# Performance work log

Hardware: AMD Instinct MI355X
Metric: run time of the kernel (lower is better)

The kernel has to match this reference:

```python
import jax, jax.numpy as jnp
import numpy as np
from jax import lax

I, H, O, L = 8, 50, 6, 3
B, T = 4096, 256


def setup_inputs() -> dict:
    key = jax.random.key(0)
    ks = jax.random.split(key, 16)
    s = 1.0 / np.sqrt(H)  # PyTorch LSTM init scale
    inp = {"x": jax.random.normal(ks[0], (B, T, I), dtype=jnp.float32)}
    in_dims = [I, H, H]
    ki = 1
    for l in range(L):
        inp[f"w_ih{l}"] = jax.random.uniform(ks[ki], (4 * H, in_dims[l]), minval=-s, maxval=s); ki += 1
        inp[f"w_hh{l}"] = jax.random.uniform(ks[ki], (4 * H, H), minval=-s, maxval=s); ki += 1
        inp[f"b_ih{l}"] = jax.random.uniform(ks[ki], (4 * H,), minval=-s, maxval=s); ki += 1
        inp[f"b_hh{l}"] = jax.random.uniform(ks[ki], (4 * H,), minval=-s, maxval=s); ki += 1
    inp["w_fc"] = jax.random.uniform(ks[13], (O, H), minval=-s, maxval=s)
    inp["b_fc"] = jax.random.uniform(ks[14], (O,), minval=-s, maxval=s)
    return inp


def _lstm_layer(x, w_ih, w_hh, b_ih, b_hh):
    # x: [B, T, in]; returns [B, T, H]. PyTorch gate order: i, f, g, o.
    b = b_ih + b_hh
    pre = jnp.einsum('bti,gi->btg', x, w_ih) + b  # input projections for all steps at once
    h0 = jnp.zeros((x.shape[0], H), x.dtype)
    c0 = jnp.zeros((x.shape[0], H), x.dtype)

    def step(carry, p_t):
        h, c = carry
        gates = p_t + h @ w_hh.T
        i, f, g, o = jnp.split(gates, 4, axis=-1)
        i = jax.nn.sigmoid(i); f = jax.nn.sigmoid(f)
        g = jnp.tanh(g); o = jax.nn.sigmoid(o)
        c = f * c + i * g
        h = o * jnp.tanh(c)
        return (h, c), h

    (_, _), hs = lax.scan(step, (h0, c0), jnp.swapaxes(pre, 0, 1))  # [T, B, H]
    return jnp.swapaxes(hs, 0, 1)


def reference(x, w_ih0, w_hh0, b_ih0, b_hh0, w_ih1, w_hh1, b_ih1, b_hh1,
              w_ih2, w_hh2, b_ih2, b_hh2, w_fc, b_fc):
    h = _lstm_layer(x, w_ih0, w_hh0, b_ih0, b_hh0)
    h = _lstm_layer(h, w_ih1, w_hh1, b_ih1, b_hh1)
    h = _lstm_layer(h, w_ih2, w_hh2, b_ih2, b_hh2)
    last = h[:, -1, :]  # [B, H]
    return last @ w_fc.T + b_fc  # [B, O]
```

## Files before the change

### kernel.cpp

```cpp
#include <hip/hip_runtime.h>
#include <hip/hip_bf16.h>
#include <cstddef>


#define T_STEPS 256
#define BTOT    4096
#define NTHR    768

typedef __attribute__((ext_vector_type(8))) short short8;
typedef __attribute__((ext_vector_type(4))) float f32x4;

#define BAR() do { \
    asm volatile("s_waitcnt lgkmcnt(0)" ::: "memory"); \
    __builtin_amdgcn_sched_barrier(0); \
    __builtin_amdgcn_s_barrier(); \
    __builtin_amdgcn_sched_barrier(0); \
} while (0)

__device__ __forceinline__ float fast_sigmoid(float x) {
    float e = __builtin_amdgcn_exp2f(-1.4426950408889634f * x);
    return __builtin_amdgcn_rcpf(1.0f + e);
}
__device__ __forceinline__ float fast_tanh(float x) {
    float e = __builtin_amdgcn_exp2f(2.8853900817779268f * x);
    return 1.0f - 2.0f * __builtin_amdgcn_rcpf(1.0f + e);
}
__device__ __forceinline__ unsigned short f2bf(float x) {
    union { __hip_bfloat16 b; unsigned short s; } u;
    u.b = __float2bfloat16(x);
    return u.s;
}
__device__ __forceinline__ float bf2f(unsigned short s) {
    union { unsigned u; float f; } v; v.u = (unsigned)s << 16; return v.f;
}
__device__ __forceinline__ float cell_upd(f32x4 g, float& cst) {
    float ig = fast_sigmoid(g[0]);
    float fg = fast_sigmoid(g[1]);
    float gg = fast_tanh(g[2]);
    float og = fast_sigmoid(g[3]);
    float c  = fmaf(fg, cst, ig * gg);
    cst = c;
    return og * fast_tanh(c);
}

template<int NT, int KS, int XK, int BIASK>
__device__ __forceinline__ void load_wb(int T0, int lane,
    const float* __restrict__ w_ih, const float* __restrict__ w_hh,
    const float* __restrict__ b_ih, const float* __restrict__ b_hh,
    short8 (&Wh)[NT][KS], short8 (&Wl)[NT][KS])
{
    const int m = lane & 15, kg = lane >> 4;
    #pragma unroll
    for (int q = 0; q < NT; ++q) {
        int gp = (T0 + q) * 16 + m;
        int gr = (gp < 200) ? ((gp & 3) * 50 + (gp >> 2)) : -1;
        #pragma unroll
        for (int ks = 0; ks < KS; ++ks)
            #pragma unroll
            for (int e = 0; e < 8; ++e) {
                int k = ks * 32 + kg * 8 + e;
                float v = 0.0f;
                if (gr >= 0) {
                    if (k < XK) v = w_ih[gr * XK + k];
                    else if (k < XK + 50) v = w_hh[gr * 50 + (k - XK)];
                    else if (k == BIASK) v = b_ih[gr] + b_hh[gr];
                }
                unsigned short hb = f2bf(v);
                Wh[q][ks][e] = (short)hb;
                Wl[q][ks][e] = (short)f2bf(v - bf2f(hb));
            }
    }
}

template<int NT, int KS, int HK, bool WRB, bool LASTL>
__device__ __forceinline__ void step_body(
    int t, int T0, int lane,
    const short* Arh,
    short* Awh,
    short* Axh,
    float* hfp,
    const short8 (&Wh)[NT][KS], const short8 (&Wl)[NT][KS],
    float (&cst)[NT])
{
    const int b = lane & 15, kg = lane >> 4;

    short8 Ah[KS];
    #pragma unroll
    for (int ks = 0; ks < KS; ++ks)
        Ah[ks] = *(const short8*)&Arh[(ks * 4 + kg) * 128 + b * 8];

    f32x4 acc[NT];
    #pragma unroll
    for (int q = 0; q < NT; ++q) acc[q] = (f32x4){0.0f, 0.0f, 0.0f, 0.0f};

    #pragma unroll
    for (int ks = 0; ks < KS; ++ks)
        #pragma unroll
        for (int q = 0; q < NT; ++q)
            acc[q] = __builtin_amdgcn_mfma_f32_16x16x32_bf16(Wh[q][ks], Ah[ks], acc[q], 0, 0, 0);
    #pragma unroll
    for (int ks = 0; ks < KS; ++ks)
        #pragma unroll
        for (int q = 0; q < NT; ++q)
            acc[q] = __builtin_amdgcn_mfma_f32_16x16x32_bf16(Wl[q][ks], Ah[ks], acc[q], 0, 0, 0);

    #pragma unroll
    for (int q = 0; q < NT; ++q) {
        int n = (T0 + q) * 4 + kg;
        if (n < 50) {
            float h = cell_upd(acc[q], cst[q]);
            unsigned short hb = f2bf(h);
            int k  = HK + n;
            Awh[(k >> 3) * 128 + b * 8 + (k & 7)] = (short)hb;
            if (WRB)
                Axh[(n >> 3) * 128 + b * 8 + (n & 7)] = (short)hb;
            if (LASTL && t == T_STEPS - 1) hfp[b * 56 + n] = h;
        }
    }
}

template<int NT, bool XST>
__device__ void role_l0(int T0, int lane, int b0, const float* __restrict__ xf,
    const float* w_ih, const float* w_hh, const float* b_ih, const float* b_hh,
    short (*A0h)[1024], short (*A1h)[2048])
{
    short8 Wh[NT][2], Wl[NT][2];
    load_wb<NT, 2, 8, 58>(T0, lane, w_ih, w_hh, b_ih, b_hh, Wh, Wl);
    float cst[NT];
    #pragma unroll
    for (int q = 0; q < NT; ++q) cst[q] = 0.0f;
    const int bb = lane & 15, kg = lane >> 4;

    for (int it = 0; it < T_STEPS + 2; ++it) {
        const bool stg = XST && (kg == 0) && (it + 1 < T_STEPS);
        float xs[8];
        if (stg) {
            const float* xr = &xf[((size_t)(b0 + bb) * T_STEPS + (it + 1)) * 8];
            *(float4*)&xs[0] = *(const float4*)xr;
            *(float4*)&xs[4] = *(const float4*)(xr + 4);
        }
        if (it < T_STEPS) {
            int cur = it & 1, nxt = cur ^ 1;
            step_body<NT, 2, 8, true, false>(it, T0, lane,
                A0h[cur], A0h[nxt], A1h[cur], nullptr, Wh, Wl, cst);
        }
        if (stg) {
            int nb = (it + 1) & 1;
            short8 hi;
            #pragma unroll
            for (int e = 0; e < 8; ++e) hi[e] = (short)f2bf(xs[e]);
            *(short8*)&A0h[nb][bb * 8] = hi;
        }
        BAR();
    }
}

template<bool LASTL>
__device__ void role_mid(int T0, int lane,
    const float* w_ih, const float* w_hh, const float* b_ih, const float* b_hh,
    short (*Arh)[2048], short (*Axh)[2048], float* hfp)
{
    constexpr int SKEW = LASTL ? 2 : 1;
    short8 Wh[3][4], Wl[3][4];
    load_wb<3, 4, 50, 100>(T0, lane, w_ih, w_hh, b_ih, b_hh, Wh, Wl);
    float cst[3] = {0.0f, 0.0f, 0.0f};

    for (int it = 0; it < T_STEPS + 2; ++it) {
        int t = it - SKEW;
        if (t >= 0 && t < T_STEPS) {
            step_body<3, 4, 50, !LASTL, LASTL>(t, T0, lane,
                Arh[t & 1], Arh[(t + 1) & 1],
                LASTL ? (short*)nullptr : Axh[t & 1],
                hfp, Wh, Wl, cst);
        }
        BAR();
    }
}

__device__ void role_orphan(int lane,
    const float* w_ih1, const float* w_hh1, const float* b_ih1, const float* b_hh1,
    const float* w_ih2, const float* w_hh2, const float* b_ih2, const float* b_hh2,
    short (*A1h)[2048], short (*A2h)[2048], float* hfp)
{
    short8 W1h[1][4], W1l[1][4], W2h[1][4], W2l[1][4];
    load_wb<1, 4, 50, 100>(12, lane, w_ih1, w_hh1, b_ih1, b_hh1, W1h, W1l);
    load_wb<1, 4, 50, 100>(12, lane, w_ih2, w_hh2, b_ih2, b_hh2, W2h, W2l);
    float c1 = 0.0f, c2 = 0.0f;
    const int b = lane & 15, kg = lane >> 4;

    for (int it = 0; it < T_STEPS + 2; ++it) {
        int t1 = it - 1, t2 = it - 2;
        bool d1 = (unsigned)t1 < T_STEPS, d2 = (unsigned)t2 < T_STEPS;

        short8 A1[4], A2[4];
        #pragma unroll
        for (int ks = 0; ks < 4; ++ks) {
            int ga = (ks * 4 + kg) * 128 + b * 8;
            if (d1) A1[ks] = *(const short8*)&A1h[t1 & 1][ga];
            if (d2) A2[ks] = *(const short8*)&A2h[t2 & 1][ga];
        }

        f32x4 a1 = (f32x4){0.0f, 0.0f, 0.0f, 0.0f};
        f32x4 a2 = (f32x4){0.0f, 0.0f, 0.0f, 0.0f};
        #pragma unroll
        for (int ks = 0; ks < 4; ++ks) {
            if (d1) a1 = __builtin_amdgcn_mfma_f32_16x16x32_bf16(W1h[0][ks], A1[ks], a1, 0, 0, 0);
            if (d2) a2 = __builtin_amdgcn_mfma_f32_16x16x32_bf16(W2h[0][ks], A2[ks], a2, 0, 0, 0);
        }
        #pragma unroll
        for (int ks = 0; ks < 4; ++ks) {
            if (d1) a1 = __builtin_amdgcn_mfma_f32_16x16x32_bf16(W1l[0][ks], A1[ks], a1, 0, 0, 0);
            if (d2) a2 = __builtin_amdgcn_mfma_f32_16x16x32_bf16(W2l[0][ks], A2[ks], a2, 0, 0, 0);
        }

        const int n = 48 + kg;
        if (d1 && kg < 2) {
            float h = cell_upd(a1, c1);
            unsigned short hb = f2bf(h);
            int k = 50 + n;
            A1h[(t1 + 1) & 1][(k >> 3) * 128 + b * 8 + (k & 7)] = (short)hb;
            A2h[t1 & 1][(n >> 3) * 128 + b * 8 + (n & 7)] = (short)hb;
        }
        if (d2 && kg < 2) {
            float h = cell_upd(a2, c2);
            unsigned short hb = f2bf(h);
            int k = 50 + n;
            A2h[(t2 + 1) & 1][(k >> 3) * 128 + b * 8 + (k & 7)] = (short)hb;
            if (t2 == T_STEPS - 1) hfp[b * 56 + n] = h;
        }
        BAR();
    }
}

__global__ __launch_bounds__(NTHR) void lstm_fused(
    const float* __restrict__ xf,
    const float* w_ih0, const float* w_hh0, const float* b_ih0, const float* b_hh0,
    const float* w_ih1, const float* w_hh1, const float* b_ih1, const float* b_hh1,
    const float* w_ih2, const float* w_hh2, const float* b_ih2, const float* b_hh2,
    const float* __restrict__ w_fc, const float* __restrict__ b_fc,
    float* __restrict__ out)
{
    __shared__ __align__(16) short A0h[2][1024];
    __shared__ __align__(16) short A1h[2][2048];
    __shared__ __align__(16) short A2h[2][2048];
    __shared__ __align__(16) float hf[16 * 56];

    const int tid  = threadIdx.x;
    const int lane = tid & 63;
    const int wid  = tid >> 6;
    const int b0   = blockIdx.x * 16;

    for (int i = tid; i < 2048; i += NTHR) ((short*)A0h)[i] = 0;
    for (int i = tid; i < 4096; i += NTHR) { ((short*)A1h)[i] = 0; ((short*)A2h)[i] = 0; }
    __syncthreads();

    if (tid < 32) {
        int buf = tid >> 4, b = tid & 15;
        A0h[buf][(58 >> 3) * 128 + b * 8 + (58 & 7)] = (short)0x3F80;
        A1h[buf][(100 >> 3) * 128 + b * 8 + (100 & 7)] = (short)0x3F80;
        A2h[buf][(100 >> 3) * 128 + b * 8 + (100 & 7)] = (short)0x3F80;
    }
    if (tid < 16) {
        int b = tid;
        #pragma unroll
        for (int j = 0; j < 8; ++j) {
            float v = xf[((size_t)(b0 + b) * T_STEPS + 0) * 8 + j];
            A0h[0][b * 8 + j] = (short)f2bf(v);
        }
    }
    __syncthreads();

    if      (wid == 0)  role_l0<5, false>(0, lane, b0, xf, w_ih0, w_hh0, b_ih0, b_hh0, A0h, A1h);
    else if (wid == 1)  role_l0<4, false>(5, lane, b0, xf, w_ih0, w_hh0, b_ih0, b_hh0, A0h, A1h);
    else if (wid == 2)  role_l0<4, true >(9, lane, b0, xf, w_ih0, w_hh0, b_ih0, b_hh0, A0h, A1h);
    else if (wid == 3)  role_mid<false>(0, lane, w_ih1, w_hh1, b_ih1, b_hh1, A1h, A2h, nullptr);
    else if (wid == 4)  role_mid<false>(3, lane, w_ih1, w_hh1, b_ih1, b_hh1, A1h, A2h, nullptr);
    else if (wid == 5)  role_mid<false>(6, lane, w_ih1, w_hh1, b_ih1, b_hh1, A1h, A2h, nullptr);
    else if (wid == 6)  role_mid<false>(9, lane, w_ih1, w_hh1, b_ih1, b_hh1, A1h, A2h, nullptr);
    else if (wid == 7)  role_mid<true >(0, lane, w_ih2, w_hh2, b_ih2, b_hh2, A2h, nullptr, hf);
    else if (wid == 8)  role_mid<true >(3, lane, w_ih2, w_hh2, b_ih2, b_hh2, A2h, nullptr, hf);
    else if (wid == 9)  role_mid<true >(6, lane, w_ih2, w_hh2, b_ih2, b_hh2, A2h, nullptr, hf);
    else if (wid == 10) role_mid<true >(9, lane, w_ih2, w_hh2, b_ih2, b_hh2, A2h, nullptr, hf);
    else                role_orphan(lane,
                            w_ih1, w_hh1, b_ih1, b_hh1,
                            w_ih2, w_hh2, b_ih2, b_hh2,
                            A1h, A2h, hf);

    __syncthreads();

    if (tid < 96) {
        int b = tid / 6, o = tid - b * 6;
        float a = b_fc[o];
        #pragma unroll
        for (int n = 0; n < 50; ++n)
            a = fmaf(w_fc[o * 50 + n], hf[b * 56 + n], a);
        out[(size_t)(b0 + b) * 6 + o] = a;
    }
}

extern "C" void kernel_launch(void* const* d_in, const int* in_sizes, int n_in,
                              void* d_out, int out_size, void* d_ws, size_t ws_size,
                              hipStream_t stream) {
    (void)in_sizes; (void)n_in; (void)d_ws; (void)ws_size; (void)out_size;

    const float* x     = (const float*)d_in[0];
    const float* w_ih0 = (const float*)d_in[1];
    const float* w_hh0 = (const float*)d_in[2];
    const float* b_ih0 = (const float*)d_in[3];
    const float* b_hh0 = (const float*)d_in[4];
    const float* w_ih1 = (const float*)d_in[5];
    const float* w_hh1 = (const float*)d_in[6];
    const float* b_ih1 = (const float*)d_in[7];
    const float* b_hh1 = (const float*)d_in[8];
    const float* w_ih2 = (const float*)d_in[9];
    const float* w_hh2 = (const float*)d_in[10];
    const float* b_ih2 = (const float*)d_in[11];
    const float* b_hh2 = (const float*)d_in[12];
    const float* w_fc  = (const float*)d_in[13];
    const float* b_fc  = (const float*)d_in[14];
    float* out = (float*)d_out;

    lstm_fused<<<dim3(BTOT / 16), dim3(NTHR), 0, stream>>>(
        x, w_ih0, w_hh0, b_ih0, b_hh0, w_ih1, w_hh1, b_ih1, b_hh1,
        w_ih2, w_hh2, b_ih2, b_hh2, w_fc, b_fc, out);
}
```

Baseline: 304.8 us.

## Single-buffer LDS state with two barriers per step and register prefetch of activations

Drops the double-buffered LDS state arrays for single buffers. Each timestep now uses two barriers: the first separates compute and writes, the second follows a register prefetch of the next step's inputs from LDS. The orphan warp now also takes one layer-0 gate tile, so layer 0 is split 4/4/4+1. The x staging is pipelined two steps ahead from global memory. This trades a second barrier per step for earlier LDS reads and halved LDS footprint, and the extra barrier may cost more than it saves.

```diff
diff --git a/kernel.cpp b/kernel.cpp
--- a/kernel.cpp
+++ b/kernel.cpp
@@ -72,37 +72,38 @@
     }
 }
 
-template<int NT, int KS, int HK, bool WRB, bool LASTL>
-__device__ __forceinline__ void step_body(
-    int t, int T0, int lane,
-    const short* Arh,
-    short* Awh,
-    short* Axh,
-    float* hfp,
+template<int KS>
+__device__ __forceinline__ void prefetch(const short* Ar, int lane, short8 (&Ap)[KS]) {
+    const int b = lane & 15, kg = lane >> 4;
+    #pragma unroll
+    for (int ks = 0; ks < KS; ++ks)
+        Ap[ks] = *(const short8*)&Ar[(ks * 4 + kg) * 128 + b * 8];
+}
+
+template<int T0, int NT, int KS, int HK, bool WRB, bool LASTL>
+__device__ __forceinline__ void compute_step(
+    int t, int lane,
+    short* Aw, short* Ax, float* hfp,
+    const short8 (&Ap)[KS],
     const short8 (&Wh)[NT][KS], const short8 (&Wl)[NT][KS],
     float (&cst)[NT])
 {
     const int b = lane & 15, kg = lane >> 4;
 
-    short8 Ah[KS];
+    f32x4 acc[NT];
+    #pragma unroll
+    for (int q = 0; q < NT; ++q) acc[q] = (f32x4){0.0f, 0.0f, 0.0f, 0.0f};
+
     #pragma unroll
     for (int ks = 0; ks < KS; ++ks)
-        Ah[ks] = *(const short8*)&Arh[(ks * 4 + kg) * 128 + b * 8];
-
-    f32x4 acc[NT];
-    #pragma unroll
-    for (int q = 0; q < NT; ++q) acc[q] = (f32x4){0.0f, 0.0f, 0.0f, 0.0f};
-
+        #pragma unroll
+        for (int q = 0; q < NT; ++q)
+            acc[q] = __builtin_amdgcn_mfma_f32_16x16x32_bf16(Wh[q][ks], Ap[ks], acc[q], 0, 0, 0);
     #pragma unroll
     for (int ks = 0; ks < KS; ++ks)
         #pragma unroll
         for (int q = 0; q < NT; ++q)
-            acc[q] = __builtin_amdgcn_mfma_f32_16x16x32_bf16(Wh[q][ks], Ah[ks], acc[q], 0, 0, 0);
-    #pragma unroll
-    for (int ks = 0; ks < KS; ++ks)
-        #pragma unroll
-        for (int q = 0; q < NT; ++q)
-            acc[q] = __builtin_amdgcn_mfma_f32_16x16x32_bf16(Wl[q][ks], Ah[ks], acc[q], 0, 0, 0);
+            acc[q] = __builtin_amdgcn_mfma_f32_16x16x32_bf16(Wl[q][ks], Ap[ks], acc[q], 0, 0, 0);
 
     #pragma unroll
     for (int q = 0; q < NT; ++q) {
@@ -110,124 +111,104 @@
         if (n < 50) {
             float h = cell_upd(acc[q], cst[q]);
             unsigned short hb = f2bf(h);
-            int k  = HK + n;
-            Awh[(k >> 3) * 128 + b * 8 + (k & 7)] = (short)hb;
+            int k = HK + n;
+            Aw[(k >> 3) * 128 + b * 8 + (k & 7)] = (short)hb;
             if (WRB)
-                Axh[(n >> 3) * 128 + b * 8 + (n & 7)] = (short)hb;
+                Ax[(n >> 3) * 128 + b * 8 + (n & 7)] = (short)hb;
             if (LASTL && t == T_STEPS - 1) hfp[b * 56 + n] = h;
         }
     }
 }
 
-template<int NT, bool XST>
-__device__ void role_l0(int T0, int lane, int b0, const float* __restrict__ xf,
+template<int T0, bool XST>
+__device__ void role_l0(int lane, int b0, const float* __restrict__ xf,
     const float* w_ih, const float* w_hh, const float* b_ih, const float* b_hh,
-    short (*A0h)[1024], short (*A1h)[2048])
-{
-    short8 Wh[NT][2], Wl[NT][2];
-    load_wb<NT, 2, 8, 58>(T0, lane, w_ih, w_hh, b_ih, b_hh, Wh, Wl);
-    float cst[NT];
-    #pragma unroll
-    for (int q = 0; q < NT; ++q) cst[q] = 0.0f;
+    short* A0, short* A1)
+{
+    short8 Wh[4][2], Wl[4][2];
+    load_wb<4, 2, 8, 58>(T0, lane, w_ih, w_hh, b_ih, b_hh, Wh, Wl);
+    float cst[4] = {0.0f, 0.0f, 0.0f, 0.0f};
+    short8 Ap[2];
     const int bb = lane & 15, kg = lane >> 4;
 
-    for (int it = 0; it < T_STEPS + 2; ++it) {
-        const bool stg = XST && (kg == 0) && (it + 1 < T_STEPS);
-        float xs[8];
-        if (stg) {
-            const float* xr = &xf[((size_t)(b0 + bb) * T_STEPS + (it + 1)) * 8];
-            *(float4*)&xs[0] = *(const float4*)xr;
-            *(float4*)&xs[4] = *(const float4*)(xr + 4);
+    float xp[2][8];
+    if (XST && kg == 0) {
+        #pragma unroll
+        for (int s = 0; s < 2; ++s) {
+            const float* xr = &xf[((size_t)(b0 + bb) * T_STEPS + (1 + s)) * 8];
+            *(float4*)&xp[s][0] = *(const float4*)xr;
+            *(float4*)&xp[s][4] = *(const float4*)(xr + 4);
         }
-        if (it < T_STEPS) {
-            int cur = it & 1, nxt = cur ^ 1;
-            step_body<NT, 2, 8, true, false>(it, T0, lane,
-                A0h[cur], A0h[nxt], A1h[cur], nullptr, Wh, Wl, cst);
+    }
+
+    for (int it = -1; it < T_STEPS + 2; ++it) {
+        if (0 <= it && it < T_STEPS)
+            compute_step<T0, 4, 2, 8, true, false>(it, lane, A0, A1, nullptr, Ap, Wh, Wl, cst);
+        if (XST && kg == 0 && it >= 0) {
+            if (it + 1 < T_STEPS) {
+                short8 hi;
+                #pragma unroll
+                for (int e = 0; e < 8; ++e) hi[e] = (short)f2bf(xp[it & 1][e]);
+                *(short8*)&A0[bb * 8] = hi;
+            }
+            if (it + 3 < T_STEPS) {
+                const float* xr = &xf[((size_t)(b0 + bb) * T_STEPS + (it + 3)) * 8];
+                *(float4*)&xp[it & 1][0] = *(const float4*)xr;
+                *(float4*)&xp[it & 1][4] = *(const float4*)(xr + 4);
+            }
         }
-        if (stg) {
-            int nb = (it + 1) & 1;
-            short8 hi;
-            #pragma unroll
-            for (int e = 0; e < 8; ++e) hi[e] = (short)f2bf(xs[e]);
-            *(short8*)&A0h[nb][bb * 8] = hi;
-        }
-        BAR();
-    }
-}
-
-template<bool LASTL>
-__device__ void role_mid(int T0, int lane,
+        BAR();
+        if (0 <= it + 1 && it + 1 < T_STEPS) prefetch<2>(A0, lane, Ap);
+        BAR();
+    }
+}
+
+template<int T0, bool LASTL>
+__device__ void role_mid(int lane,
     const float* w_ih, const float* w_hh, const float* b_ih, const float* b_hh,
-    short (*Arh)[2048], short (*Axh)[2048], float* hfp)
+    short* Ar, short* Ax, float* hfp)
 {
     constexpr int SKEW = LASTL ? 2 : 1;
     short8 Wh[3][4], Wl[3][4];
     load_wb<3, 4, 50, 100>(T0, lane, w_ih, w_hh, b_ih, b_hh, Wh, Wl);
     float cst[3] = {0.0f, 0.0f, 0.0f};
-
-    for (int it = 0; it < T_STEPS + 2; ++it) {
+    short8 Ap[4];
+
+    for (int it = -1; it < T_STEPS + 2; ++it) {
         int t = it - SKEW;
-        if (t >= 0 && t < T_STEPS) {
-            step_body<3, 4, 50, !LASTL, LASTL>(t, T0, lane,
-                Arh[t & 1], Arh[(t + 1) & 1],
-                LASTL ? (short*)nullptr : Axh[t & 1],
-                hfp, Wh, Wl, cst);
-        }
+        if (0 <= t && t < T_STEPS)
+            compute_step<T0, 3, 4, 50, !LASTL, LASTL>(t, lane, Ar, Ax, hfp, Ap, Wh, Wl, cst);
+        BAR();
+        if (0 <= t + 1 && t + 1 < T_STEPS) prefetch<4>(Ar, lane, Ap);
         BAR();
     }
 }
 
 __device__ void role_orphan(int lane,
+    const float* w_ih0, const float* w_hh0, const float* b_ih0, const float* b_hh0,
     const float* w_ih1, const float* w_hh1, const float* b_ih1, const float* b_hh1,
     const float* w_ih2, const float* w_hh2, const float* b_ih2, const float* b_hh2,
-    short (*A1h)[2048], short (*A2h)[2048], float* hfp)
-{
-    short8 W1h[1][4], W1l[1][4], W2h[1][4], W2l[1][4];
+    short* A0, short* A1, short* A2, float* hfp)
+{
+    short8 W0h[1][2], W0l[1][2], W1h[1][4], W1l[1][4], W2h[1][4], W2l[1][4];
+    load_wb<1, 2, 8, 58>(12, lane, w_ih0, w_hh0, b_ih0, b_hh0, W0h, W0l);
     load_wb<1, 4, 50, 100>(12, lane, w_ih1, w_hh1, b_ih1, b_hh1, W1h, W1l);
     load_wb<1, 4, 50, 100>(12, lane, w_ih2, w_hh2, b_ih2, b_hh2, W2h, W2l);
-    float c1 = 0.0f, c2 = 0.0f;
-    const int b = lane & 15, kg = lane >> 4;
-
-    for (int it = 0; it < T_STEPS + 2; ++it) {
-        int t1 = it - 1, t2 = it - 2;
-        bool d1 = (unsigned)t1 < T_STEPS, d2 = (unsigned)t2 < T_STEPS;
-
-        short8 A1[4], A2[4];
-        #pragma unroll
-        for (int ks = 0; ks < 4; ++ks) {
-            int ga = (ks * 4 + kg) * 128 + b * 8;
-            if (d1) A1[ks] = *(const short8*)&A1h[t1 & 1][ga];
-            if (d2) A2[ks] = *(const short8*)&A2h[t2 & 1][ga];
-        }
-
-        f32x4 a1 = (f32x4){0.0f, 0.0f, 0.0f, 0.0f};
-        f32x4 a2 = (f32x4){0.0f, 0.0f, 0.0f, 0.0f};
-        #pragma unroll
-        for (int ks = 0; ks < 4; ++ks) {
-            if (d1) a1 = __builtin_amdgcn_mfma_f32_16x16x32_bf16(W1h[0][ks], A1[ks], a1, 0, 0, 0);
-            if (d2) a2 = __builtin_amdgcn_mfma_f32_16x16x32_bf16(W2h[0][ks], A2[ks], a2, 0, 0, 0);
-        }
-        #pragma unroll
-        for (int ks = 0; ks < 4; ++ks) {
-            if (d1) a1 = __builtin_amdgcn_mfma_f32_16x16x32_bf16(W1l[0][ks], A1[ks], a1, 0, 0, 0);
-            if (d2) a2 = __builtin_amdgcn_mfma_f32_16x16x32_bf16(W2l[0][ks], A2[ks], a2, 0, 0, 0);
-        }
-
-        const int n = 48 + kg;
-        if (d1 && kg < 2) {
-            float h = cell_upd(a1, c1);
-            unsigned short hb = f2bf(h);
-            int k = 50 + n;
-            A1h[(t1 + 1) & 1][(k >> 3) * 128 + b * 8 + (k & 7)] = (short)hb;
-            A2h[t1 & 1][(n >> 3) * 128 + b * 8 + (n & 7)] = (short)hb;
-        }
-        if (d2 && kg < 2) {
-            float h = cell_upd(a2, c2);
-            unsigned short hb = f2bf(h);
-            int k = 50 + n;
-            A2h[(t2 + 1) & 1][(k >> 3) * 128 + b * 8 + (k & 7)] = (short)hb;
-            if (t2 == T_STEPS - 1) hfp[b * 56 + n] = h;
-        }
+    float c0[1] = {0.0f}, c1[1] = {0.0f}, c2[1] = {0.0f};
+    short8 Ap0[2], Ap1[4], Ap2[4];
+
+    for (int it = -1; it < T_STEPS + 2; ++it) {
+        int t0 = it, t1 = it - 1, t2 = it - 2;
+        if (0 <= t0 && t0 < T_STEPS)
+            compute_step<12, 1, 2, 8, true, false>(t0, lane, A0, A1, nullptr, Ap0, W0h, W0l, c0);
+        if (0 <= t1 && t1 < T_STEPS)
+            compute_step<12, 1, 4, 50, true, false>(t1, lane, A1, A2, nullptr, Ap1, W1h, W1l, c1);
+        if (0 <= t2 && t2 < T_STEPS)
+            compute_step<12, 1, 4, 50, false, true>(t2, lane, A2, nullptr, hfp, Ap2, W2h, W2l, c2);
+        BAR();
+        if (t0 + 1 >= 0 && t0 + 1 < T_STEPS) prefetch<2>(A0, lane, Ap0);
+        if (t1 + 1 >= 0 && t1 + 1 < T_STEPS) prefetch<4>(A1, lane, Ap1);
+        if (t2 + 1 >= 0 && t2 + 1 < T_STEPS) prefetch<4>(A2, lane, Ap2);
         BAR();
     }
 }
@@ -240,9 +221,9 @@
     const float* __restrict__ w_fc, const float* __restrict__ b_fc,
     float* __restrict__ out)
 {
-    __shared__ __align__(16) short A0h[2][1024];
-    __shared__ __align__(16) short A1h[2][2048];
-    __shared__ __align__(16) short A2h[2][2048];
+    __shared__ __align__(16) short A0[1024];
+    __shared__ __align__(16) short A1[2048];
+    __shared__ __align__(16) short A2[2048];
     __shared__ __align__(16) float hf[16 * 56];
 
     const int tid  = threadIdx.x;
@@ -250,41 +231,39 @@
     const int wid  = tid >> 6;
     const int b0   = blockIdx.x * 16;
 
-    for (int i = tid; i < 2048; i += NTHR) ((short*)A0h)[i] = 0;
-    for (int i = tid; i < 4096; i += NTHR) { ((short*)A1h)[i] = 0; ((short*)A2h)[i] = 0; }
+    for (int i = tid; i < 1024; i += NTHR) A0[i] = 0;
+    for (int i = tid; i < 2048; i += NTHR) { A1[i] = 0; A2[i] = 0; }
     __syncthreads();
 
-    if (tid < 32) {
-        int buf = tid >> 4, b = tid & 15;
-        A0h[buf][(58 >> 3) * 128 + b * 8 + (58 & 7)] = (short)0x3F80;
-        A1h[buf][(100 >> 3) * 128 + b * 8 + (100 & 7)] = (short)0x3F80;
-        A2h[buf][(100 >> 3) * 128 + b * 8 + (100 & 7)] = (short)0x3F80;
-    }
     if (tid < 16) {
         int b = tid;
+        A0[7 * 128 + b * 8 + 2]  = (short)0x3F80;
+        A1[12 * 128 + b * 8 + 4] = (short)0x3F80;
+        A2[12 * 128 + b * 8 + 4] = (short)0x3F80;
         #pragma unroll
         for (int j = 0; j < 8; ++j) {
             float v = xf[((size_t)(b0 + b) * T_STEPS + 0) * 8 + j];
-            A0h[0][b * 8 + j] = (short)f2bf(v);
+            A0[b * 8 + j] = (short)f2bf(v);
         }
     }
     __syncthreads();
 
-    if      (wid == 0)  role_l0<5, false>(0, lane, b0, xf, w_ih0, w_hh0, b_ih0, b_hh0, A0h, A1h);
-    else if (wid == 1)  role_l0<4, false>(5, lane, b0, xf, w_ih0, w_hh0, b_ih0, b_hh0, A0h, A1h);
-    else if (wid == 2)  role_l0<4, true >(9, lane, b0, xf, w_ih0, w_hh0, b_ih0, b_hh0, A0h, A1h);
-    else if (wid == 3)  role_mid<false>(0, lane, w_ih1, w_hh1, b_ih1, b_hh1, A1h, A2h, nullptr);
-    else if (wid == 4)  role_mid<false>(3, lane, w_ih1, w_hh1, b_ih1, b_hh1, A1h, A2h, nullptr);
-    else if (wid == 5)  role_mid<false>(6, lane, w_ih1, w_hh1, b_ih1, b_hh1, A1h, A2h, nullptr);
-    else if (wid == 6)  role_mid<false>(9, lane, w_ih1, w_hh1, b_ih1, b_hh1, A1h, A2h, nullptr);
-    else if (wid == 7)  role_mid<true >(0, lane, w_ih2, w_hh2, b_ih2, b_hh2, A2h, nullptr, hf);
-    else if (wid == 8)  role_mid<true >(3, lane, w_ih2, w_hh2, b_ih2, b_hh2, A2h, nullptr, hf);
-    else if (wid == 9)  role_mid<true >(6, lane, w_ih2, w_hh2, b_ih2, b_hh2, A2h, nullptr, hf);
-    else if (wid == 10) role_mid<true >(9, lane, w_ih2, w_hh2, b_ih2, b_hh2, A2h, nullptr, hf);
+    if      (wid == 0)  role_l0<0, false>(lane, b0, xf, w_ih0, w_hh0, b_ih0, b_hh0, A0, A1);
+    else if (wid == 1)  role_l0<4, false>(lane, b0, xf, w_ih0, w_hh0, b_ih0, b_hh0, A0, A1);
+    else if (wid == 2)  role_l0<8, true >(lane, b0, xf, w_ih0, w_hh0, b_ih0, b_hh0, A0, A1);
+    else if (wid == 3)  role_mid<0, false>(lane, w_ih1, w_hh1, b_ih1, b_hh1, A1, A2, nullptr);
+    else if (wid == 4)  role_mid<3, false>(lane, w_ih1, w_hh1, b_ih1, b_hh1, A1, A2, nullptr);
+    else if (wid == 5)  role_mid<6, false>(lane, w_ih1, w_hh1, b_ih1, b_hh1, A1, A2, nullptr);
+    else if (wid == 6)  role_mid<9, false>(lane, w_ih1, w_hh1, b_ih1, b_hh1, A1, A2, nullptr);
+    else if (wid == 7)  role_mid<0, true >(lane, w_ih2, w_hh2, b_ih2, b_hh2, A2, nullptr, hf);
+    else if (wid == 8)  role_mid<3, true >(lane, w_ih2, w_hh2, b_ih2, b_hh2, A2, nullptr, hf);
+    else if (wid == 9)  role_mid<6, true >(lane, w_ih2, w_hh2, b_ih2, b_hh2, A2, nullptr, hf);
+    else if (wid == 10) role_mid<9, true >(lane, w_ih2, w_hh2, b_ih2, b_hh2, A2, nullptr, hf);
     else                role_orphan(lane,
+                            w_ih0, w_hh0, b_ih0, b_hh0,
                             w_ih1, w_hh1, b_ih1, b_hh1,
                             w_ih2, w_hh2, b_ih2, b_hh2,
-                            A1h, A2h, hf);
+                            A0, A1, A2, hf);
 
     __syncthreads();
 
```

Result: slower. 329.6 us (+8.2%).
